# Performance work log

Hardware: AMD Instinct MI355X
Metric: run time of the kernel (lower is better)

## Reference

```python
import jax, jax.numpy as jnp
import numpy as np

CHAMFER_WEIGHT = 1.0
REG_WEIGHT = 0.1


def setup_inputs() -> dict:
    key = jax.random.key(0)
    k1, k2, k3 = jax.random.split(key, 3)
    B, N, M, K = 16, 4096, 4096, 64
    return {
        "predicted_points": jax.random.normal(k1, (B, N, 3), dtype=jnp.float32),
        "ground_truth_points": jax.random.normal(k2, (B, M, 3), dtype=jnp.float32),
        "trans_feat": jax.random.normal(k3, (B, K, K), dtype=jnp.float32),
    }


def _chamfer(pred, target):
    # Euclidean (non-squared) pairwise distances, matching torch.cdist.
    # Gram trick avoids materializing [B,N,M,3].
    p2 = jnp.sum(pred * pred, axis=-1)          # [B,N]
    t2 = jnp.sum(target * target, axis=-1)      # [B,M]
    cross = jnp.einsum("bnd,bmd->bnm", pred, target)  # [B,N,M]
    d2 = p2[:, :, None] + t2[:, None, :] - 2.0 * cross
    dist = jnp.sqrt(jnp.maximum(d2, 0.0))       # [B,N,M]
    min1 = jnp.min(dist, axis=2)                # [B,N] pred -> nearest target
    min2 = jnp.min(dist, axis=1)                # [B,M] target -> nearest pred
    return jnp.mean(jnp.mean(min1, axis=1) + jnp.mean(min2, axis=1))


def _feature_transform_reg(trans):
    K = trans.shape[1]
    I = jnp.eye(K, dtype=trans.dtype)
    gram = jnp.einsum("bik,bjk->bij", trans, trans)  # trans @ trans^T
    # Frobenius norm per batch element, then mean over batch
    return jnp.mean(jnp.sqrt(jnp.sum((gram - I) ** 2, axis=(1, 2))))


def reference(predicted_points, ground_truth_points, trans_feat):
    chamfer = _chamfer(predicted_points, ground_truth_points)
    reg = _feature_transform_reg(trans_feat)
    return CHAMFER_WEIGHT * chamfer + REG_WEIGHT * reg
```

## Files before the change

kernel.cpp:

```cpp
#include <hip/hip_runtime.h>
#include <math.h>

#define BB 16
#define NN 4096
#define MM 4096
#define NSLICE 2
#define SLICE_COLS 2048
#define NJT (SLICE_COLS / 64)
#define ROWS_PER_WAVE 128
#define ROWS_PER_BLOCK 512
#define NROWS_TOTAL (2 * BB * NN)
#define NCHAMFER 512
#define EPW 4352

typedef __attribute__((ext_vector_type(8))) short bf16x8;
typedef __attribute__((ext_vector_type(16))) float f32x16;

static __device__ inline unsigned short f2bf(float f) {
    unsigned int u = __float_as_uint(f);
    return (unsigned short)((u + 0x7FFFu + ((u >> 16) & 1u)) >> 16);
}
static __device__ inline bf16x8 bzero() {
    bf16x8 z;
    #pragma unroll
    for (int i = 0; i < 8; ++i) z[i] = 0;
    return z;
}
static __device__ inline f32x16 fzero16() {
    f32x16 z;
    #pragma unroll
    for (int i = 0; i < 16; ++i) z[i] = 0.f;
    return z;
}

#define MFMA32(Af, Bf, Cf) __builtin_amdgcn_mfma_f32_32x32x16_bf16(Af, Bf, Cf, 0, 0, 0)
#define MINC(F, X1, X2)                                                  \
    do {                                                                 \
        _Pragma("unroll")                                                \
        for (int r = 0; r < 16; ++r)                                     \
            mv[F][r] = fminf(fminf((X1)[r], (X2)[r]), mv[F][r]);         \
    } while (0)

__global__ __launch_bounds__(256, 2) void chamfer_min_kernel(
    const float* __restrict__ pred, const float* __restrict__ gt,
    const float* __restrict__ trans, float* __restrict__ wsmin,
    float* __restrict__ out)
{
    const int bx  = blockIdx.x;
    const int tid = threadIdx.x;

    if (bx >= NCHAMFER) {
        if (tid < 64) {
            const int b = bx - NCHAMFER;
            const int lane = tid;
            const int hi = lane >> 5, li = lane & 31;
            const float* T = trans + (size_t)b * 64 * 64;
            bf16x8 frag[2][4];
            #pragma unroll
            for (int h = 0; h < 2; ++h)
                #pragma unroll
                for (int s = 0; s < 4; ++s) {
                    const float* rp = T + (size_t)(h * 32 + li) * 64 + s * 16 + hi * 8;
                    const float4 u0 = *(const float4*)rp;
                    const float4 u1 = *(const float4*)(rp + 4);
                    bf16x8 fr;
                    fr[0] = (short)f2bf(u0.x); fr[1] = (short)f2bf(u0.y);
                    fr[2] = (short)f2bf(u0.z); fr[3] = (short)f2bf(u0.w);
                    fr[4] = (short)f2bf(u1.x); fr[5] = (short)f2bf(u1.y);
                    fr[6] = (short)f2bf(u1.z); fr[7] = (short)f2bf(u1.w);
                    frag[h][s] = fr;
                }
            float fsum = 0.f;
            #pragma unroll
            for (int fi = 0; fi < 2; ++fi)
                #pragma unroll
                for (int fj = 0; fj < 2; ++fj) {
                    f32x16 a = fzero16();
                    #pragma unroll
                    for (int s = 0; s < 4; ++s)
                        a = MFMA32(frag[fi][s], frag[fj][s], a);
                    #pragma unroll
                    for (int r = 0; r < 16; ++r) {
                        const int row = fi * 32 + (r & 3) + 8 * (r >> 2) + 4 * hi;
                        const int col = fj * 32 + li;
                        const float d = a[r] - ((row == col) ? 1.0f : 0.0f);
                        fsum = fmaf(d, d, fsum);
                    }
                }
            #pragma unroll
            for (int off = 32; off > 0; off >>= 1)
                fsum += __shfl_down(fsum, off, 64);
            if (lane == 0)
                atomicAdd(out, (0.1f / (float)BB) * sqrtf(fsum));
        }
        return;
    }

    __shared__ __align__(16) float smem[4 * EPW];

    const int lane = tid & 63;
    const int w    = tid >> 6;
    const int li   = lane & 31;
    const int hi   = lane >> 5;
    const int tile   = bx & 7;
    const int mslice = (bx >> 3) & 1;
    const int b      = (bx >> 4) & 15;
    const int dir    = bx >> 8;
    const float* rows = dir ? gt : pred;
    const float* cols = dir ? pred : gt;
    const float* rb = rows + (size_t)b * NN * 3;
    const float* cb = cols + ((size_t)b * MM + (size_t)mslice * SLICE_COLS) * 3;

    const int rbase = tile * ROWS_PER_BLOCK + w * ROWS_PER_WAVE;
    bf16x8 A0 = bzero(), A1 = bzero(), A2 = bzero(), A3 = bzero();
    if (lane < 32) {
        #pragma unroll
        for (int f = 0; f < 4; ++f) {
            const float* rp = rb + (size_t)(rbase + f * 32 + li) * 3;
            const float px = rp[0], py = rp[1], pz = rp[2];
            const float p2 = px * px + py * py + pz * pz;
            bf16x8 fr = bzero();
            fr[0] = (short)f2bf(-2.f * px);
            fr[1] = (short)f2bf(-2.f * py);
            fr[2] = (short)f2bf(-2.f * pz);
            fr[3] = (short)f2bf(p2);
            fr[4] = (short)0x3F80;
            if (f == 0) A0 = fr; else if (f == 1) A1 = fr;
            else if (f == 2) A2 = fr; else A3 = fr;
        }
    }

    uint4* sB = (uint4*)smem;
    #pragma unroll
    for (int i = 0; i < SLICE_COLS / 256; ++i) {
        const int c = i * 256 + tid;
        const float* tp = cb + (size_t)c * 3;
        const float tx = tp[0], ty = tp[1], tz = tp[2];
        const float t2 = tx * tx + ty * ty + tz * tz;
        uint4 pk;
        pk.x = (unsigned)f2bf(tx) | ((unsigned)f2bf(ty) << 16);
        pk.y = (unsigned)f2bf(tz) | (0x3F80u << 16);
        pk.z = (unsigned)f2bf(t2);
        pk.w = 0u;
        sB[c] = pk;
    }
    __syncthreads();

    float mv[4][16];
    #pragma unroll
    for (int f = 0; f < 4; ++f)
        #pragma unroll
        for (int r = 0; r < 16; ++r) mv[f][r] = 3.4e38f;

    const f32x16 Z = fzero16();
    const bf16x8* sBf = (const bf16x8*)smem;

    bf16x8 c1 = sBf[li], c2 = sBf[32 + li];
    bf16x8 b1, b2;
    f32x16 pa1 = MFMA32(A0, c1, Z), pa2 = MFMA32(A0, c2, Z);
    f32x16 ca1, ca2;

    for (int jt = 0; jt < NJT - 1; ++jt) {
        b1 = sBf[(jt + 1) * 64 + li];
        b2 = sBf[(jt + 1) * 64 + 32 + li];
        ca1 = MFMA32(A1, c1, Z); ca2 = MFMA32(A1, c2, Z);
        MINC(0, pa1, pa2);
        pa1 = MFMA32(A2, c1, Z); pa2 = MFMA32(A2, c2, Z);
        MINC(1, ca1, ca2);
        ca1 = MFMA32(A3, c1, Z); ca2 = MFMA32(A3, c2, Z);
        MINC(2, pa1, pa2);
        c1 = b1; c2 = b2;
        pa1 = MFMA32(A0, c1, Z); pa2 = MFMA32(A0, c2, Z);
        MINC(3, ca1, ca2);
    }
    ca1 = MFMA32(A1, c1, Z); ca2 = MFMA32(A1, c2, Z);
    MINC(0, pa1, pa2);
    pa1 = MFMA32(A2, c1, Z); pa2 = MFMA32(A2, c2, Z);
    MINC(1, ca1, ca2);
    ca1 = MFMA32(A3, c1, Z); ca2 = MFMA32(A3, c2, Z);
    MINC(2, pa1, pa2);
    MINC(3, ca1, ca2);

    __syncthreads();
    {
        float* base = smem + w * EPW + li * 136;
        #pragma unroll
        for (int f = 0; f < 4; ++f)
            #pragma unroll
            for (int q = 0; q < 4; ++q) {
                const int rowl = f * 32 + q * 8 + hi * 4;
                *(float4*)&base[rowl] =
                    make_float4(mv[f][4*q], mv[f][4*q+1], mv[f][4*q+2], mv[f][4*q+3]);
            }
    }
    __syncthreads();

    #pragma unroll
    for (int half = 0; half < 2; ++half) {
        const int x = half * 256 + tid;
        const int wsrc = x >> 7;
        const int rl = x & 127;
        const float* rb2 = smem + wsrc * EPW + rl;
        float m = 3.4e38f;
        #pragma unroll
        for (int c = 0; c < 32; ++c) m = fminf(m, rb2[c * 136]);
        wsmin[(size_t)mslice * NROWS_TOTAL + (size_t)(dir * BB + b) * NN
              + tile * ROWS_PER_BLOCK + x] = m;
    }
}

__global__ __launch_bounds__(256) void chamfer_finish_kernel(
    const float* __restrict__ wsmin, float* __restrict__ out)
{
    const int tid = threadIdx.x;
    const int g = blockIdx.x * 256 + tid;
    const float v = fminf(wsmin[g], wsmin[NROWS_TOTAL + g]);
    float d = sqrtf(fmaxf(v, 0.0f));
    #pragma unroll
    for (int off = 32; off > 0; off >>= 1)
        d += __shfl_down(d, off, 64);
    __shared__ float ssum[4];
    if ((tid & 63) == 0) ssum[tid >> 6] = d;
    __syncthreads();
    if (tid == 0) {
        const float s = ssum[0] + ssum[1] + ssum[2] + ssum[3];
        atomicAdd(out, s * (1.0f / ((float)BB * (float)NN)));
    }
}

extern "C" void kernel_launch(void* const* d_in, const int* in_sizes, int n_in,
                              void* d_out, int out_size, void* d_ws, size_t ws_size,
                              hipStream_t stream)
{
    const float* pred  = (const float*)d_in[0];
    const float* gt    = (const float*)d_in[1];
    const float* trans = (const float*)d_in[2];
    float* out = (float*)d_out;
    float* wsmin = (float*)d_ws;

    hipMemsetAsync(out, 0, sizeof(float), stream);
    chamfer_min_kernel<<<dim3(NCHAMFER + BB), dim3(256), 0, stream>>>(
        pred, gt, trans, wsmin, out);
    chamfer_finish_kernel<<<dim3(NROWS_TOTAL / 256), dim3(256), 0, stream>>>(
        wsmin, out);
}
```

Baseline: 32.92 us.

## Halve rows per wave, double blocks and occupancy, simplify MFMA loop

Each wave now handles 64 rows (two A fragments) instead of 128, so the chamfer grid doubles to 1024 blocks and launch bounds rise to 4 blocks per SM. The software-pipelined MFMA/min loop is replaced by a plain loop of four MFMAs per column tile, and the column staging loads two points per thread with float2 reads. The reg-loss block also loads fragments lazily to cut register use. The aim is more waves and more latency hiding, at the cost of staging the column slice into LDS twice as often and losing the explicit overlap of MFMA with the min reductions.

```diff
diff --git a/kernel.cpp b/kernel.cpp
--- a/kernel.cpp
+++ b/kernel.cpp
@@ -7,11 +7,11 @@
 #define NSLICE 2
 #define SLICE_COLS 2048
 #define NJT (SLICE_COLS / 64)
-#define ROWS_PER_WAVE 128
-#define ROWS_PER_BLOCK 512
+#define ROWS_PER_WAVE 64
+#define ROWS_PER_BLOCK 256
 #define NROWS_TOTAL (2 * BB * NN)
-#define NCHAMFER 512
-#define EPW 4352
+#define NCHAMFER 1024
+#define EPW 2176
 
 typedef __attribute__((ext_vector_type(8))) short bf16x8;
 typedef __attribute__((ext_vector_type(16))) float f32x16;
@@ -34,14 +34,8 @@
 }
 
 #define MFMA32(Af, Bf, Cf) __builtin_amdgcn_mfma_f32_32x32x16_bf16(Af, Bf, Cf, 0, 0, 0)
-#define MINC(F, X1, X2)                                                  \
-    do {                                                                 \
-        _Pragma("unroll")                                                \
-        for (int r = 0; r < 16; ++r)                                     \
-            mv[F][r] = fminf(fminf((X1)[r], (X2)[r]), mv[F][r]);         \
-    } while (0)
-
-__global__ __launch_bounds__(256, 2) void chamfer_min_kernel(
+
+__global__ __launch_bounds__(256, 4) void chamfer_min_kernel(
     const float* __restrict__ pred, const float* __restrict__ gt,
     const float* __restrict__ trans, float* __restrict__ wsmin,
     float* __restrict__ out)
@@ -55,12 +49,13 @@
             const int lane = tid;
             const int hi = lane >> 5, li = lane & 31;
             const float* T = trans + (size_t)b * 64 * 64;
-            bf16x8 frag[2][4];
+            float fsum = 0.f;
             #pragma unroll
-            for (int h = 0; h < 2; ++h)
+            for (int fi = 0; fi < 2; ++fi) {
+                bf16x8 fa[4];
                 #pragma unroll
                 for (int s = 0; s < 4; ++s) {
-                    const float* rp = T + (size_t)(h * 32 + li) * 64 + s * 16 + hi * 8;
+                    const float* rp = T + (size_t)(fi * 32 + li) * 64 + s * 16 + hi * 8;
                     const float4 u0 = *(const float4*)rp;
                     const float4 u1 = *(const float4*)(rp + 4);
                     bf16x8 fr;
@@ -68,17 +63,23 @@
                     fr[2] = (short)f2bf(u0.z); fr[3] = (short)f2bf(u0.w);
                     fr[4] = (short)f2bf(u1.x); fr[5] = (short)f2bf(u1.y);
                     fr[6] = (short)f2bf(u1.z); fr[7] = (short)f2bf(u1.w);
-                    frag[h][s] = fr;
+                    fa[s] = fr;
                 }
-            float fsum = 0.f;
-            #pragma unroll
-            for (int fi = 0; fi < 2; ++fi)
                 #pragma unroll
                 for (int fj = 0; fj < 2; ++fj) {
                     f32x16 a = fzero16();
                     #pragma unroll
-                    for (int s = 0; s < 4; ++s)
-                        a = MFMA32(frag[fi][s], frag[fj][s], a);
+                    for (int s = 0; s < 4; ++s) {
+                        const float* rp = T + (size_t)(fj * 32 + li) * 64 + s * 16 + hi * 8;
+                        const float4 u0 = *(const float4*)rp;
+                        const float4 u1 = *(const float4*)(rp + 4);
+                        bf16x8 fr;
+                        fr[0] = (short)f2bf(u0.x); fr[1] = (short)f2bf(u0.y);
+                        fr[2] = (short)f2bf(u0.z); fr[3] = (short)f2bf(u0.w);
+                        fr[4] = (short)f2bf(u1.x); fr[5] = (short)f2bf(u1.y);
+                        fr[6] = (short)f2bf(u1.z); fr[7] = (short)f2bf(u1.w);
+                        a = MFMA32(fa[s], fr, a);
+                    }
                     #pragma unroll
                     for (int r = 0; r < 16; ++r) {
                         const int row = fi * 32 + (r & 3) + 8 * (r >> 2) + 4 * hi;
@@ -87,6 +88,7 @@
                         fsum = fmaf(d, d, fsum);
                     }
                 }
+            }
             #pragma unroll
             for (int off = 32; off > 0; off >>= 1)
                 fsum += __shfl_down(fsum, off, 64);
@@ -102,20 +104,20 @@
     const int w    = tid >> 6;
     const int li   = lane & 31;
     const int hi   = lane >> 5;
-    const int tile   = bx & 7;
-    const int mslice = (bx >> 3) & 1;
-    const int b      = (bx >> 4) & 15;
-    const int dir    = bx >> 8;
+    const int tile   = bx & 15;
+    const int mslice = (bx >> 4) & 1;
+    const int b      = (bx >> 5) & 15;
+    const int dir    = bx >> 9;
     const float* rows = dir ? gt : pred;
     const float* cols = dir ? pred : gt;
     const float* rb = rows + (size_t)b * NN * 3;
     const float* cb = cols + ((size_t)b * MM + (size_t)mslice * SLICE_COLS) * 3;
 
     const int rbase = tile * ROWS_PER_BLOCK + w * ROWS_PER_WAVE;
-    bf16x8 A0 = bzero(), A1 = bzero(), A2 = bzero(), A3 = bzero();
+    bf16x8 A0 = bzero(), A1 = bzero();
     if (lane < 32) {
         #pragma unroll
-        for (int f = 0; f < 4; ++f) {
+        for (int f = 0; f < 2; ++f) {
             const float* rp = rb + (size_t)(rbase + f * 32 + li) * 3;
             const float px = rp[0], py = rp[1], pz = rp[2];
             const float p2 = px * px + py * py + pz * pz;
@@ -125,88 +127,73 @@
             fr[2] = (short)f2bf(-2.f * pz);
             fr[3] = (short)f2bf(p2);
             fr[4] = (short)0x3F80;
-            if (f == 0) A0 = fr; else if (f == 1) A1 = fr;
-            else if (f == 2) A2 = fr; else A3 = fr;
+            if (f == 0) A0 = fr; else A1 = fr;
         }
     }
 
     uint4* sB = (uint4*)smem;
     #pragma unroll
-    for (int i = 0; i < SLICE_COLS / 256; ++i) {
-        const int c = i * 256 + tid;
-        const float* tp = cb + (size_t)c * 3;
-        const float tx = tp[0], ty = tp[1], tz = tp[2];
-        const float t2 = tx * tx + ty * ty + tz * tz;
-        uint4 pk;
-        pk.x = (unsigned)f2bf(tx) | ((unsigned)f2bf(ty) << 16);
-        pk.y = (unsigned)f2bf(tz) | (0x3F80u << 16);
-        pk.z = (unsigned)f2bf(t2);
-        pk.w = 0u;
-        sB[c] = pk;
-    }
-    __syncthreads();
-
-    float mv[4][16];
-    #pragma unroll
-    for (int f = 0; f < 4; ++f)
-        #pragma unroll
-        for (int r = 0; r < 16; ++r) mv[f][r] = 3.4e38f;
+    for (int i = 0; i < SLICE_COLS / 512; ++i) {
+        const int c0 = i * 512 + 2 * tid;
+        const float2* sp = (const float2*)(cb + (size_t)c0 * 3);
+        const float2 v0 = sp[0], v1 = sp[1], v2 = sp[2];
+        const float t2a = v0.x * v0.x + v0.y * v0.y + v1.x * v1.x;
+        const float t2b = v1.y * v1.y + v2.x * v2.x + v2.y * v2.y;
+        uint4 pa, pb;
+        pa.x = (unsigned)f2bf(v0.x) | ((unsigned)f2bf(v0.y) << 16);
+        pa.y = (unsigned)f2bf(v1.x) | (0x3F80u << 16);
+        pa.z = (unsigned)f2bf(t2a);
+        pa.w = 0u;
+        pb.x = (unsigned)f2bf(v1.y) | ((unsigned)f2bf(v2.x) << 16);
+        pb.y = (unsigned)f2bf(v2.y) | (0x3F80u << 16);
+        pb.z = (unsigned)f2bf(t2b);
+        pb.w = 0u;
+        sB[c0]     = pa;
+        sB[c0 + 1] = pb;
+    }
+    __syncthreads();
+
+    float mv0[16], mv1[16];
+    #pragma unroll
+    for (int r = 0; r < 16; ++r) { mv0[r] = 3.4e38f; mv1[r] = 3.4e38f; }
 
     const f32x16 Z = fzero16();
     const bf16x8* sBf = (const bf16x8*)smem;
 
-    bf16x8 c1 = sBf[li], c2 = sBf[32 + li];
-    bf16x8 b1, b2;
-    f32x16 pa1 = MFMA32(A0, c1, Z), pa2 = MFMA32(A0, c2, Z);
-    f32x16 ca1, ca2;
-
-    for (int jt = 0; jt < NJT - 1; ++jt) {
-        b1 = sBf[(jt + 1) * 64 + li];
-        b2 = sBf[(jt + 1) * 64 + 32 + li];
-        ca1 = MFMA32(A1, c1, Z); ca2 = MFMA32(A1, c2, Z);
-        MINC(0, pa1, pa2);
-        pa1 = MFMA32(A2, c1, Z); pa2 = MFMA32(A2, c2, Z);
-        MINC(1, ca1, ca2);
-        ca1 = MFMA32(A3, c1, Z); ca2 = MFMA32(A3, c2, Z);
-        MINC(2, pa1, pa2);
-        c1 = b1; c2 = b2;
-        pa1 = MFMA32(A0, c1, Z); pa2 = MFMA32(A0, c2, Z);
-        MINC(3, ca1, ca2);
-    }
-    ca1 = MFMA32(A1, c1, Z); ca2 = MFMA32(A1, c2, Z);
-    MINC(0, pa1, pa2);
-    pa1 = MFMA32(A2, c1, Z); pa2 = MFMA32(A2, c2, Z);
-    MINC(1, ca1, ca2);
-    ca1 = MFMA32(A3, c1, Z); ca2 = MFMA32(A3, c2, Z);
-    MINC(2, pa1, pa2);
-    MINC(3, ca1, ca2);
+    for (int jt = 0; jt < NJT; ++jt) {
+        const bf16x8 c1 = sBf[jt * 64 + li];
+        const bf16x8 c2 = sBf[jt * 64 + 32 + li];
+        f32x16 a0 = MFMA32(A0, c1, Z);
+        f32x16 a1 = MFMA32(A0, c2, Z);
+        f32x16 a2 = MFMA32(A1, c1, Z);
+        f32x16 a3 = MFMA32(A1, c2, Z);
+        #pragma unroll
+        for (int r = 0; r < 16; ++r)
+            mv0[r] = fminf(fminf(a0[r], a1[r]), mv0[r]);
+        #pragma unroll
+        for (int r = 0; r < 16; ++r)
+            mv1[r] = fminf(fminf(a2[r], a3[r]), mv1[r]);
+    }
 
     __syncthreads();
     {
-        float* base = smem + w * EPW + li * 136;
-        #pragma unroll
-        for (int f = 0; f < 4; ++f)
-            #pragma unroll
-            for (int q = 0; q < 4; ++q) {
-                const int rowl = f * 32 + q * 8 + hi * 4;
-                *(float4*)&base[rowl] =
-                    make_float4(mv[f][4*q], mv[f][4*q+1], mv[f][4*q+2], mv[f][4*q+3]);
-            }
-    }
-    __syncthreads();
-
-    #pragma unroll
-    for (int half = 0; half < 2; ++half) {
-        const int x = half * 256 + tid;
-        const int wsrc = x >> 7;
-        const int rl = x & 127;
-        const float* rb2 = smem + wsrc * EPW + rl;
-        float m = 3.4e38f;
-        #pragma unroll
-        for (int c = 0; c < 32; ++c) m = fminf(m, rb2[c * 136]);
-        wsmin[(size_t)mslice * NROWS_TOTAL + (size_t)(dir * BB + b) * NN
-              + tile * ROWS_PER_BLOCK + x] = m;
-    }
+        float* wb = smem + w * EPW + li * 68;
+        #pragma unroll
+        for (int q = 0; q < 4; ++q) {
+            const int rl = q * 8 + hi * 4;
+            *(float4*)&wb[rl]      = make_float4(mv0[4*q], mv0[4*q+1], mv0[4*q+2], mv0[4*q+3]);
+            *(float4*)&wb[rl + 32] = make_float4(mv1[4*q], mv1[4*q+1], mv1[4*q+2], mv1[4*q+3]);
+        }
+    }
+    __syncthreads();
+
+    const int wsrc = tid >> 6, rl = tid & 63;
+    const float* rb2 = smem + wsrc * EPW + rl;
+    float m = 3.4e38f;
+    #pragma unroll
+    for (int c = 0; c < 32; ++c) m = fminf(m, rb2[c * 68]);
+    wsmin[(size_t)mslice * NROWS_TOTAL + (size_t)(dir * BB + b) * NN
+          + tile * ROWS_PER_BLOCK + tid] = m;
 }
 
 __global__ __launch_bounds__(256) void chamfer_finish_kernel(
```

Measured after the change: 33.18 us. About the same (+0.8%).
